# Performance work log

Hardware: AMD Instinct MI355X
Metric: run time of the kernel (lower is better)

## Reference

```python
import jax, jax.numpy as jnp
import numpy as np

EPS = 1e-8

def _affine_combine(prev, curr):
    # compose affine maps: (a2,b2) o (a1,b1) = (a2*a1, a2*b1 + b2)
    a1, b1 = prev
    a2, b2 = curr
    return a2 * a1, a2 * b1 + b2

def parallel_scan_log(coeffs, values):
    # h_t = a_t * h_{t-1} + b_t  (inclusive scan along seq axis)
    a = jnp.clip(coeffs, EPS, 1.0 - EPS)
    _, h = jax.lax.associative_scan(_affine_combine, (a, values), axis=1)
    return h

def setup_inputs() -> dict:
    key = jax.random.key(0)
    kx, kz, kh = jax.random.split(key, 3)
    B, S, D, H = 4, 8192, 512, 512
    scale = 1.0 / np.sqrt(D)
    return {
        "x": jax.random.normal(kx, (B, S, D), dtype=jnp.float32),
        "W_z": jax.random.normal(kz, (H, D), dtype=jnp.float32) * scale,
        "b_z": jnp.zeros((H,), dtype=jnp.float32),
        "W_h": jax.random.normal(kh, (H, D), dtype=jnp.float32) * scale,
        "b_h": jnp.zeros((H,), dtype=jnp.float32),
    }

def reference(x, W_z, b_z, W_h, b_h):
    # z_t gates, h_tilde candidate; recurrence h_t = (1-z_t)*h_{t-1} + z_t*h~_t
    z = jax.nn.sigmoid(jnp.einsum("bsd,hd->bsh", x, W_z) + b_z)
    h_tilde = jnp.tanh(jnp.einsum("bsd,hd->bsh", x, W_h) + b_h)
    return parallel_scan_log(1.0 - z, z * h_tilde)
```

## Files before the change

kernel.cpp:

```cpp
#include <hip/hip_runtime.h>
#include <hip/hip_bf16.h>
#include <hip/hip_fp16.h>
#include <cstdint>
#include <cstddef>

typedef __bf16 bf16;
typedef __bf16 bf16x8 __attribute__((ext_vector_type(8)));
typedef float f32x4 __attribute__((ext_vector_type(4)));

static constexpr int NB = 4;
static constexpr int S  = 8192;
static constexpr int D  = 512;
static constexpr int H  = 512;
static constexpr int M  = NB * S;
static constexpr int CH = 64;
static constexpr int NC = S / CH;

#define BM 128
#define BN 128
#define BK 64

__device__ __forceinline__ void ld_lds16(void* lds, const void* g) {
  __builtin_amdgcn_global_load_lds(
      (const __attribute__((address_space(1))) uint32_t*)g,
      (__attribute__((address_space(3))) uint32_t*)lds, 16, 0, 0);
}

__global__ void cvt_w(const float* __restrict__ Wz, bf16* __restrict__ Wzb,
                      const float* __restrict__ Wh, bf16* __restrict__ Whb) {
  int idx = blockIdx.x * blockDim.x + threadIdx.x;
  const int per = H * (D / 8);
  const float* src; bf16* dst;
  if (idx < per) { src = Wz; dst = Wzb; }
  else           { src = Wh; dst = Whb; idx -= per; }
  const int row = idx >> 6;
  const int blk = idx & 63;
  const float* s = src + (size_t)row * D + blk * 8;
  const float4 f0 = *(const float4*)s;
  const float4 f1 = *(const float4*)(s + 4);
  bf16x8 o;
  o[0] = (bf16)f0.x; o[1] = (bf16)f0.y; o[2] = (bf16)f0.z; o[3] = (bf16)f0.w;
  o[4] = (bf16)f1.x; o[5] = (bf16)f1.y; o[6] = (bf16)f1.z; o[7] = (bf16)f1.w;
  const int dblk = blk ^ (row & 7);
  *(bf16x8*)(dst + (size_t)row * D + dblk * 8) = o;
}

__global__ __launch_bounds__(256, 2)
void gemm_gates(const float* __restrict__ Xf,
                const bf16* __restrict__ Wzb,
                const bf16* __restrict__ Whb,
                const float* __restrict__ bz,
                const float* __restrict__ bh,
                __half2* __restrict__ AB,
                float* __restrict__ cA,
                float* __restrict__ cB) {
  __shared__ __attribute__((aligned(16))) bf16 As[BM * BK];
  __shared__ __attribute__((aligned(16))) bf16 Zs[BN * BK];
  __shared__ __attribute__((aligned(16))) bf16 Hs[BN * BK];

  const int bid = blockIdx.x;
  const int swz = (bid & 7) * 128 + (bid >> 3);
  const int mt = swz >> 2;
  const int nt = swz & 3;
  const int m0 = mt * BM;
  const int n0 = nt * BN;
  const int tid = threadIdx.x;
  const int wave = tid >> 6;
  const int lane = tid & 63;
  const int wr = wave >> 1;
  const int wc = wave & 1;
  const int lr = lane & 15;
  const int lk = lane >> 4;
  const int xk = (lr & 7) << 3;

  float4 xr[4][2];
  const int sx_row = (tid * 8 + 0) >> 6;

  f32x4 accz[4][4], acch[4][4];
  const f32x4 vzero = {0.f, 0.f, 0.f, 0.f};
#pragma unroll
  for (int i = 0; i < 4; ++i)
#pragma unroll
    for (int j = 0; j < 4; ++j) { accz[i][j] = vzero; acch[i][j] = vzero; }

#pragma unroll
  for (int it = 0; it < 4; ++it) {
    const int idx = it * 256 + tid;
    const int row = idx >> 3;
    const int grp = idx & 7;
    const float* gp = Xf + (size_t)(m0 + row) * D + grp * 8;
    xr[it][0] = *(const float4*)gp;
    xr[it][1] = *(const float4*)(gp + 4);
  }

  for (int ks = 0; ks < D / BK; ++ks) {
#pragma unroll
    for (int it = 0; it < 4; ++it) {
      const int idx = it * 256 + tid;
      const int row = idx >> 3;
      const int grp = idx & 7;
      bf16x8 o;
      o[0] = (bf16)xr[it][0].x; o[1] = (bf16)xr[it][0].y;
      o[2] = (bf16)xr[it][0].z; o[3] = (bf16)xr[it][0].w;
      o[4] = (bf16)xr[it][1].x; o[5] = (bf16)xr[it][1].y;
      o[6] = (bf16)xr[it][1].z; o[7] = (bf16)xr[it][1].w;
      *(bf16x8*)&As[row * BK + ((grp ^ (row & 7)) << 3)] = o;
    }
#pragma unroll
    for (int it = 0; it < 4; ++it) {
      const int fb = it * 256 + wave * 64;
      const int f  = fb + lane;
      const int row = f >> 3;
      const int kc  = f & 7;
      const size_t gk = (size_t)ks * BK + kc * 8;
      ld_lds16(&Zs[(size_t)fb * 8], Wzb + (size_t)(n0 + row) * D + gk);
      ld_lds16(&Hs[(size_t)fb * 8], Whb + (size_t)(n0 + row) * D + gk);
    }
    __syncthreads();

    if (ks < D / BK - 1) {
#pragma unroll
      for (int it = 0; it < 4; ++it) {
        const int idx = it * 256 + tid;
        const int row = idx >> 3;
        const int grp = idx & 7;
        const float* gp = Xf + (size_t)(m0 + row) * D + (ks + 1) * BK + grp * 8;
        xr[it][0] = *(const float4*)gp;
        xr[it][1] = *(const float4*)(gp + 4);
      }
    }

#pragma unroll
    for (int kk = 0; kk < 2; ++kk) {
      bf16x8 af[4], zf[4], hf[4];
      const int col = (kk * 32 + lk * 8) ^ xk;
#pragma unroll
      for (int m = 0; m < 4; ++m)
        af[m] = *(const bf16x8*)&As[(wr * 64 + m * 16 + lr) * BK + col];
#pragma unroll
      for (int n = 0; n < 4; ++n) {
        const int c = (wc * 64 + n * 16 + lr) * BK + col;
        zf[n] = *(const bf16x8*)&Zs[c];
        hf[n] = *(const bf16x8*)&Hs[c];
      }
#pragma unroll
      for (int m = 0; m < 4; ++m)
#pragma unroll
        for (int n = 0; n < 4; ++n) {
          accz[m][n] = __builtin_amdgcn_mfma_f32_16x16x32_bf16(af[m], zf[n], accz[m][n], 0, 0, 0);
          acch[m][n] = __builtin_amdgcn_mfma_f32_16x16x32_bf16(af[m], hf[n], acch[m][n], 0, 0, 0);
        }
    }
    __syncthreads();
  }

  const int cg = (m0 >> 6) + wr;
  float bzv[4], bhv[4], At[4], Bt[4];
#pragma unroll
  for (int n = 0; n < 4; ++n) {
    const int gn = n0 + wc * 64 + n * 16 + lr;
    bzv[n] = bz[gn];
    bhv[n] = bh[gn];
    At[n] = 1.f;
    Bt[n] = 0.f;
  }
#pragma unroll
  for (int m = 0; m < 4; ++m) {
#pragma unroll
    for (int n = 0; n < 4; ++n) {
      const int gn = n0 + wc * 64 + n * 16 + lr;
      float Aseg = 1.f, Bseg = 0.f;
#pragma unroll
      for (int j = 0; j < 4; ++j) {
        const int gm = m0 + wr * 64 + m * 16 + lk * 4 + j;
        const float vz = accz[m][n][j] + bzv[n];
        const float vh = acch[m][n][j] + bhv[n];
        const float z = 1.f / (1.f + __expf(-vz));
        const float e = __expf(-2.f * fabsf(vh));
        float th = (1.f - e) / (1.f + e);
        th = (vh < 0.f) ? -th : th;
        float a = 1.f - z;
        a = fminf(fmaxf(a, 1e-8f), 1.f - 1e-8f);
        const float bb = z * th;
        __half2 pk;
        pk.x = __float2half_rn(a);
        pk.y = __float2half_rn(bb);
        AB[(size_t)gm * H + gn] = pk;
        Aseg = a * Aseg;
        Bseg = a * Bseg + bb;
      }
      float pa = __shfl_xor(Aseg, 16);
      float pb = __shfl_xor(Bseg, 16);
      if (lane & 16) { Bseg = Aseg * pb + Bseg; Aseg = Aseg * pa; }
      else           { Bseg = pa * Bseg + pb;   Aseg = pa * Aseg; }
      pa = __shfl_xor(Aseg, 32);
      pb = __shfl_xor(Bseg, 32);
      if (lane & 32) { Bseg = Aseg * pb + Bseg; Aseg = Aseg * pa; }
      else           { Bseg = pa * Bseg + pb;   Aseg = pa * Aseg; }
      Bt[n] = Aseg * Bt[n] + Bseg;
      At[n] = Aseg * At[n];
    }
  }
  if (lk == 0) {
#pragma unroll
    for (int n = 0; n < 4; ++n) {
      const int gn = n0 + wc * 64 + n * 16 + lr;
      const size_t so = (size_t)cg * H + gn;
      cA[so] = At[n];
      cB[so] = Bt[n];
    }
  }
}

__global__ __launch_bounds__(256)
void scan_summary(const float* __restrict__ cA,
                  const float* __restrict__ cB,
                  float* __restrict__ pref) {
  const int w = blockIdx.x * 4 + (threadIdx.x >> 6);
  const int lane = threadIdx.x & 63;
  const int b = w >> 9, h = w & (H - 1);
  float hin = 0.f;
#pragma unroll
  for (int seg = 0; seg < 2; ++seg) {
    const int c = seg * 64 + lane;
    const size_t so = ((size_t)b * NC + c) * H + h;
    float A = cA[so], Bv = cB[so];
#pragma unroll
    for (int d = 1; d < 64; d <<= 1) {
      const float pa = __shfl_up(A, d);
      const float pb = __shfl_up(Bv, d);
      if (lane >= d) { Bv = A * pb + Bv; A = A * pa; }
    }
    float eA = __shfl_up(A, 1);
    float eB = __shfl_up(Bv, 1);
    if (lane == 0) { eA = 1.f; eB = 0.f; }
    pref[so] = eA * hin + eB;
    const float tA = __shfl(A, 63);
    const float tB = __shfl(Bv, 63);
    hin = tA * hin + tB;
  }
}

__global__ __launch_bounds__(512)
void scan_apply(const __half2* __restrict__ AB, float* __restrict__ out,
                const float* __restrict__ pref) {
  const int blk = blockIdx.x;
  const int b = blk / NC, c = blk % NC;
  const int h = threadIdx.x;
  const size_t base = ((size_t)b * S + (size_t)c * CH) * H + h;
  float hcur = pref[((size_t)b * NC + c) * H + h];
#pragma unroll 4
  for (int t = 0; t < CH; ++t) {
    const size_t off = base + (size_t)t * H;
    const float2 f = __half22float2(AB[off]);
    hcur = f.x * hcur + f.y;
    out[off] = hcur;
  }
}

extern "C" void kernel_launch(void* const* d_in, const int* in_sizes, int n_in,
                              void* d_out, int out_size, void* d_ws, size_t ws_size,
                              hipStream_t stream) {
  const float* x  = (const float*)d_in[0];
  const float* Wz = (const float*)d_in[1];
  const float* bz = (const float*)d_in[2];
  const float* Wh = (const float*)d_in[3];
  const float* bh = (const float*)d_in[4];
  float* out = (float*)d_out;

  char* ws = (char*)d_ws;
  __half2* AB = (__half2*)ws;
  bf16*  Wzb  = (bf16*)(ws + (size_t)67108864);
  bf16*  Whb  = (bf16*)(ws + (size_t)67633152);
  float* cA   = (float*)(ws + (size_t)68157440);
  float* cB   = (float*)(ws + (size_t)69206016);
  float* pref = (float*)(ws + (size_t)70254592);

  cvt_w<<<2 * H * (D / 8) / 256, 256, 0, stream>>>(Wz, Wzb, Wh, Whb);
  gemm_gates<<<(M / BM) * (H / BN), 256, 0, stream>>>(x, Wzb, Whb, bz, bh,
                                                      AB, cA, cB);
  scan_summary<<<NB * H / 4, 256, 0, stream>>>(cA, cB, pref);
  scan_apply<<<NB * NC, H, 0, stream>>>(AB, out, pref);
}
```

Measured before the change: 91.58 us.

## Double-buffer weight tiles in LDS to overlap loads with MFMA compute

Splits the Z and H weight tiles into two LDS buffers and issues the async global-to-LDS loads for the next K step before computing on the current one, with the X register prefetch moved alongside. The K loop is fully unrolled. The aim is to hide weight-load latency behind the MFMA work. In exchange, LDS use grows from 48KB to 80KB per block, which may cut occupancy below the two blocks per CU the launch bounds request.

```diff
diff --git a/kernel.cpp b/kernel.cpp
--- a/kernel.cpp
+++ b/kernel.cpp
@@ -55,8 +55,10 @@
                 float* __restrict__ cA,
                 float* __restrict__ cB) {
   __shared__ __attribute__((aligned(16))) bf16 As[BM * BK];
-  __shared__ __attribute__((aligned(16))) bf16 Zs[BN * BK];
-  __shared__ __attribute__((aligned(16))) bf16 Hs[BN * BK];
+  __shared__ __attribute__((aligned(16))) bf16 Zs0[BN * BK];
+  __shared__ __attribute__((aligned(16))) bf16 Zs1[BN * BK];
+  __shared__ __attribute__((aligned(16))) bf16 Hs0[BN * BK];
+  __shared__ __attribute__((aligned(16))) bf16 Hs1[BN * BK];
 
   const int bid = blockIdx.x;
   const int swz = (bid & 7) * 128 + (bid >> 3);
@@ -74,7 +76,6 @@
   const int xk = (lr & 7) << 3;
 
   float4 xr[4][2];
-  const int sx_row = (tid * 8 + 0) >> 6;
 
   f32x4 accz[4][4], acch[4][4];
   const f32x4 vzero = {0.f, 0.f, 0.f, 0.f};
@@ -83,17 +84,18 @@
 #pragma unroll
     for (int j = 0; j < 4; ++j) { accz[i][j] = vzero; acch[i][j] = vzero; }
 
-#pragma unroll
-  for (int it = 0; it < 4; ++it) {
-    const int idx = it * 256 + tid;
-    const int row = idx >> 3;
-    const int grp = idx & 7;
-    const float* gp = Xf + (size_t)(m0 + row) * D + grp * 8;
-    xr[it][0] = *(const float4*)gp;
-    xr[it][1] = *(const float4*)(gp + 4);
-  }
-
-  for (int ks = 0; ks < D / BK; ++ks) {
+  auto loadX = [&](int ks) {
+#pragma unroll
+    for (int it = 0; it < 4; ++it) {
+      const int idx = it * 256 + tid;
+      const int row = idx >> 3;
+      const int grp = idx & 7;
+      const float* gp = Xf + (size_t)(m0 + row) * D + ks * BK + grp * 8;
+      xr[it][0] = *(const float4*)gp;
+      xr[it][1] = *(const float4*)(gp + 4);
+    }
+  };
+  auto writeX = [&]() {
 #pragma unroll
     for (int it = 0; it < 4; ++it) {
       const int idx = it * 256 + tid;
@@ -106,6 +108,8 @@
       o[6] = (bf16)xr[it][1].z; o[7] = (bf16)xr[it][1].w;
       *(bf16x8*)&As[row * BK + ((grp ^ (row & 7)) << 3)] = o;
     }
+  };
+  auto stageW = [&](int ks, bf16* Zd, bf16* Hd) {
 #pragma unroll
     for (int it = 0; it < 4; ++it) {
       const int fb = it * 256 + wave * 64;
@@ -113,23 +117,11 @@
       const int row = f >> 3;
       const int kc  = f & 7;
       const size_t gk = (size_t)ks * BK + kc * 8;
-      ld_lds16(&Zs[(size_t)fb * 8], Wzb + (size_t)(n0 + row) * D + gk);
-      ld_lds16(&Hs[(size_t)fb * 8], Whb + (size_t)(n0 + row) * D + gk);
-    }
-    __syncthreads();
-
-    if (ks < D / BK - 1) {
-#pragma unroll
-      for (int it = 0; it < 4; ++it) {
-        const int idx = it * 256 + tid;
-        const int row = idx >> 3;
-        const int grp = idx & 7;
-        const float* gp = Xf + (size_t)(m0 + row) * D + (ks + 1) * BK + grp * 8;
-        xr[it][0] = *(const float4*)gp;
-        xr[it][1] = *(const float4*)(gp + 4);
-      }
-    }
-
+      ld_lds16(&Zd[(size_t)fb * 8], Wzb + (size_t)(n0 + row) * D + gk);
+      ld_lds16(&Hd[(size_t)fb * 8], Whb + (size_t)(n0 + row) * D + gk);
+    }
+  };
+  auto compute = [&](const bf16* Zc, const bf16* Hc) {
 #pragma unroll
     for (int kk = 0; kk < 2; ++kk) {
       bf16x8 af[4], zf[4], hf[4];
@@ -140,8 +132,8 @@
 #pragma unroll
       for (int n = 0; n < 4; ++n) {
         const int c = (wc * 64 + n * 16 + lr) * BK + col;
-        zf[n] = *(const bf16x8*)&Zs[c];
-        hf[n] = *(const bf16x8*)&Hs[c];
+        zf[n] = *(const bf16x8*)&Zc[c];
+        hf[n] = *(const bf16x8*)&Hc[c];
       }
 #pragma unroll
       for (int m = 0; m < 4; ++m)
@@ -151,6 +143,20 @@
           acch[m][n] = __builtin_amdgcn_mfma_f32_16x16x32_bf16(af[m], hf[n], acch[m][n], 0, 0, 0);
         }
     }
+  };
+
+  loadX(0);
+  stageW(0, Zs0, Hs0);
+
+#pragma unroll
+  for (int ks = 0; ks < D / BK; ++ks) {
+    writeX();
+    __syncthreads();
+    if (ks < D / BK - 1) {
+      stageW(ks + 1, (ks & 1) ? Zs0 : Zs1, (ks & 1) ? Hs0 : Hs1);
+      loadX(ks + 1);
+    }
+    compute((ks & 1) ? Zs1 : Zs0, (ks & 1) ? Hs1 : Hs0);
     __syncthreads();
   }
 
```

Result: slower. 114.1 us (+24.6%).

## Keep full-K weight tiles resident in LDS and feed X directly into MFMA registers

Applied to the files above, without the earlier changes.

The GEMM block shape changes to 256x64 and the whole 64x512 slice of both weight matrices is loaded into LDS once, so the per-k-step barrier is gone. Each wave now loads its own X rows straight from global memory into registers, converts them to bf16 and uses them as MFMA A-fragments, which removes the X staging through LDS. In exchange each block uses 128KB of LDS, occupancy drops to one block per CU, and global X loads are strided rows with less coalescing. There is also less reuse, since each X row is now reloaded for 8 N-tiles instead of 4.

```diff
diff --git a/kernel.cpp b/kernel.cpp
--- a/kernel.cpp
+++ b/kernel.cpp
@@ -16,9 +16,9 @@
 static constexpr int CH = 64;
 static constexpr int NC = S / CH;
 
-#define BM 128
-#define BN 128
-#define BK 64
+#define BM 256
+#define BN 64
+#define KSTEPS 16
 
 __device__ __forceinline__ void ld_lds16(void* lds, const void* g) {
   __builtin_amdgcn_global_load_lds(
@@ -45,7 +45,7 @@
   *(bf16x8*)(dst + (size_t)row * D + dblk * 8) = o;
 }
 
-__global__ __launch_bounds__(256, 2)
+__global__ __launch_bounds__(256, 1)
 void gemm_gates(const float* __restrict__ Xf,
                 const bf16* __restrict__ Wzb,
                 const bf16* __restrict__ Whb,
@@ -54,27 +54,42 @@
                 __half2* __restrict__ AB,
                 float* __restrict__ cA,
                 float* __restrict__ cB) {
-  __shared__ __attribute__((aligned(16))) bf16 As[BM * BK];
-  __shared__ __attribute__((aligned(16))) bf16 Zs[BN * BK];
-  __shared__ __attribute__((aligned(16))) bf16 Hs[BN * BK];
+  __shared__ __attribute__((aligned(16))) bf16 Zs[64 * 512];
+  __shared__ __attribute__((aligned(16))) bf16 Hs[64 * 512];
 
   const int bid = blockIdx.x;
   const int swz = (bid & 7) * 128 + (bid >> 3);
-  const int mt = swz >> 2;
-  const int nt = swz & 3;
+  const int mt = swz >> 3;
+  const int nt = swz & 7;
   const int m0 = mt * BM;
   const int n0 = nt * BN;
   const int tid = threadIdx.x;
   const int wave = tid >> 6;
   const int lane = tid & 63;
-  const int wr = wave >> 1;
-  const int wc = wave & 1;
+  const int wr = wave;
   const int lr = lane & 15;
   const int lk = lane >> 4;
-  const int xk = (lr & 7) << 3;
+
+  const float* xbase = Xf + (size_t)(m0 + wr * 64 + lr) * D + lk * 8;
 
   float4 xr[4][2];
-  const int sx_row = (tid * 8 + 0) >> 6;
+#pragma unroll
+  for (int m = 0; m < 4; ++m) {
+    const float* gp = xbase + (size_t)m * 16 * D;
+    xr[m][0] = *(const float4*)gp;
+    xr[m][1] = *(const float4*)(gp + 4);
+  }
+
+#pragma unroll
+  for (int it = 0; it < 16; ++it) {
+    const int fb = it * 256 + wave * 64;
+    const int f  = fb + lane;
+    const int row = f >> 6;
+    const int kc  = f & 63;
+    ld_lds16(&Zs[(size_t)fb * 8], Wzb + (size_t)(n0 + row) * D + kc * 8);
+    ld_lds16(&Hs[(size_t)fb * 8], Whb + (size_t)(n0 + row) * D + kc * 8);
+  }
+  __syncthreads();
 
   f32x4 accz[4][4], acch[4][4];
   const f32x4 vzero = {0.f, 0.f, 0.f, 0.f};
@@ -84,81 +99,47 @@
     for (int j = 0; j < 4; ++j) { accz[i][j] = vzero; acch[i][j] = vzero; }
 
 #pragma unroll
-  for (int it = 0; it < 4; ++it) {
-    const int idx = it * 256 + tid;
-    const int row = idx >> 3;
-    const int grp = idx & 7;
-    const float* gp = Xf + (size_t)(m0 + row) * D + grp * 8;
-    xr[it][0] = *(const float4*)gp;
-    xr[it][1] = *(const float4*)(gp + 4);
-  }
-
-  for (int ks = 0; ks < D / BK; ++ks) {
-#pragma unroll
-    for (int it = 0; it < 4; ++it) {
-      const int idx = it * 256 + tid;
-      const int row = idx >> 3;
-      const int grp = idx & 7;
+  for (int kt = 0; kt < KSTEPS; ++kt) {
+    bf16x8 af[4];
+#pragma unroll
+    for (int m = 0; m < 4; ++m) {
       bf16x8 o;
-      o[0] = (bf16)xr[it][0].x; o[1] = (bf16)xr[it][0].y;
-      o[2] = (bf16)xr[it][0].z; o[3] = (bf16)xr[it][0].w;
-      o[4] = (bf16)xr[it][1].x; o[5] = (bf16)xr[it][1].y;
-      o[6] = (bf16)xr[it][1].z; o[7] = (bf16)xr[it][1].w;
-      *(bf16x8*)&As[row * BK + ((grp ^ (row & 7)) << 3)] = o;
-    }
-#pragma unroll
-    for (int it = 0; it < 4; ++it) {
-      const int fb = it * 256 + wave * 64;
-      const int f  = fb + lane;
-      const int row = f >> 3;
-      const int kc  = f & 7;
-      const size_t gk = (size_t)ks * BK + kc * 8;
-      ld_lds16(&Zs[(size_t)fb * 8], Wzb + (size_t)(n0 + row) * D + gk);
-      ld_lds16(&Hs[(size_t)fb * 8], Whb + (size_t)(n0 + row) * D + gk);
-    }
-    __syncthreads();
-
-    if (ks < D / BK - 1) {
-#pragma unroll
-      for (int it = 0; it < 4; ++it) {
-        const int idx = it * 256 + tid;
-        const int row = idx >> 3;
-        const int grp = idx & 7;
-        const float* gp = Xf + (size_t)(m0 + row) * D + (ks + 1) * BK + grp * 8;
-        xr[it][0] = *(const float4*)gp;
-        xr[it][1] = *(const float4*)(gp + 4);
+      o[0] = (bf16)xr[m][0].x; o[1] = (bf16)xr[m][0].y;
+      o[2] = (bf16)xr[m][0].z; o[3] = (bf16)xr[m][0].w;
+      o[4] = (bf16)xr[m][1].x; o[5] = (bf16)xr[m][1].y;
+      o[6] = (bf16)xr[m][1].z; o[7] = (bf16)xr[m][1].w;
+      af[m] = o;
+    }
+    if (kt < KSTEPS - 1) {
+#pragma unroll
+      for (int m = 0; m < 4; ++m) {
+        const float* gp = xbase + (size_t)m * 16 * D + (kt + 1) * 32;
+        xr[m][0] = *(const float4*)gp;
+        xr[m][1] = *(const float4*)(gp + 4);
       }
     }
-
-#pragma unroll
-    for (int kk = 0; kk < 2; ++kk) {
-      bf16x8 af[4], zf[4], hf[4];
-      const int col = (kk * 32 + lk * 8) ^ xk;
-#pragma unroll
-      for (int m = 0; m < 4; ++m)
-        af[m] = *(const bf16x8*)&As[(wr * 64 + m * 16 + lr) * BK + col];
+    bf16x8 zf[4], hf[4];
+#pragma unroll
+    for (int n = 0; n < 4; ++n) {
+      const int row = n * 16 + lr;
+      const int blk = (kt * 4 + lk) ^ (lr & 7);
+      zf[n] = *(const bf16x8*)&Zs[row * 512 + blk * 8];
+      hf[n] = *(const bf16x8*)&Hs[row * 512 + blk * 8];
+    }
+#pragma unroll
+    for (int m = 0; m < 4; ++m)
 #pragma unroll
       for (int n = 0; n < 4; ++n) {
-        const int c = (wc * 64 + n * 16 + lr) * BK + col;
-        zf[n] = *(const bf16x8*)&Zs[c];
-        hf[n] = *(const bf16x8*)&Hs[c];
+        accz[m][n] = __builtin_amdgcn_mfma_f32_16x16x32_bf16(af[m], zf[n], accz[m][n], 0, 0, 0);
+        acch[m][n] = __builtin_amdgcn_mfma_f32_16x16x32_bf16(af[m], hf[n], acch[m][n], 0, 0, 0);
       }
-#pragma unroll
-      for (int m = 0; m < 4; ++m)
-#pragma unroll
-        for (int n = 0; n < 4; ++n) {
-          accz[m][n] = __builtin_amdgcn_mfma_f32_16x16x32_bf16(af[m], zf[n], accz[m][n], 0, 0, 0);
-          acch[m][n] = __builtin_amdgcn_mfma_f32_16x16x32_bf16(af[m], hf[n], acch[m][n], 0, 0, 0);
-        }
-    }
-    __syncthreads();
   }
 
   const int cg = (m0 >> 6) + wr;
   float bzv[4], bhv[4], At[4], Bt[4];
 #pragma unroll
   for (int n = 0; n < 4; ++n) {
-    const int gn = n0 + wc * 64 + n * 16 + lr;
+    const int gn = n0 + n * 16 + lr;
     bzv[n] = bz[gn];
     bhv[n] = bh[gn];
     At[n] = 1.f;
@@ -168,7 +149,7 @@
   for (int m = 0; m < 4; ++m) {
 #pragma unroll
     for (int n = 0; n < 4; ++n) {
-      const int gn = n0 + wc * 64 + n * 16 + lr;
+      const int gn = n0 + n * 16 + lr;
       float Aseg = 1.f, Bseg = 0.f;
 #pragma unroll
       for (int j = 0; j < 4; ++j) {
@@ -204,7 +185,7 @@
   if (lk == 0) {
 #pragma unroll
     for (int n = 0; n < 4; ++n) {
-      const int gn = n0 + wc * 64 + n * 16 + lr;
+      const int gn = n0 + n * 16 + lr;
       const size_t so = (size_t)cg * H + gn;
       cA[so] = At[n];
       cB[so] = Bt[n];
```

New measurement: 152.2 us. 66.2% more time.
